# Kernel optimization log

Hardware: AMD Instinct MI355X
Metric: run time of the kernel (lower is better)

## Reference

```python
import jax, jax.numpy as jnp
import numpy as np

B, C, H, W = 2, 256, 64, 64
NUM_HEADS = 4
HEAD_DIM = C // NUM_HEADS
N = H * W


def setup_inputs() -> dict:
    key = jax.random.key(0)
    ks = jax.random.split(key, 10)
    x = jax.random.normal(ks[0], (B, C, H, W), dtype=jnp.float32)
    # mostly-True mask; diagonal forced True so every row has a valid key
    m = jax.random.uniform(ks[1], (B, N, N)) > 0.1
    spatial_mask = m | jnp.eye(N, dtype=bool)[None]
    s = 1.0 / np.sqrt(C)
    wq = jax.random.normal(ks[2], (C, C), dtype=jnp.float32) * s
    bq = jnp.zeros((C,), jnp.float32)
    wk = jax.random.normal(ks[3], (C, C), dtype=jnp.float32) * s
    bk = jnp.zeros((C,), jnp.float32)
    wv = jax.random.normal(ks[4], (C, C), dtype=jnp.float32) * s
    bv = jnp.zeros((C,), jnp.float32)
    # torch zero-inits out_proj; use random weights for a non-trivial baseline
    wo = jax.random.normal(ks[5], (C, C), dtype=jnp.float32) * s
    bo = jnp.zeros((C,), jnp.float32)
    return {"x": x, "spatial_mask": spatial_mask, "wq": wq, "bq": bq,
            "wk": wk, "bk": bk, "wv": wv, "bv": bv, "wo": wo, "bo": bo}


def reference(x, spatial_mask, wq, bq, wk, bk, wv, bv, wo, bo):
    b, c, h, w = x.shape
    n = h * w
    nh, hd = NUM_HEADS, HEAD_DIM
    scale = hd ** -0.5
    x_flat = x.reshape(b, c, n).transpose(0, 2, 1)           # [b, n, c]
    q = (x_flat @ wq.T + bq).reshape(b, n, nh, hd).transpose(0, 2, 1, 3)
    k = (x_flat @ wk.T + bk).reshape(b, n, nh, hd).transpose(0, 2, 1, 3)
    v = (x_flat @ wv.T + bv).reshape(b, n, nh, hd).transpose(0, 2, 1, 3)
    logits = jnp.einsum('bhqd,bhkd->bhqk', q, k) * scale      # [b, nh, n, n]
    logits = jnp.where(spatial_mask[:, None], logits, -jnp.inf)
    attn = jax.nn.softmax(logits, axis=-1)                    # dropout = identity (eval)
    out = jnp.einsum('bhqk,bhkd->bhqd', attn, v)              # [b, nh, n, hd]
    out = out.transpose(0, 2, 1, 3).reshape(b, n, c)
    out = out @ wo.T + bo
    return out.transpose(0, 2, 1).reshape(b, c, h, w)
```

## Files before the change

kernel.cpp:

```cpp
#include <hip/hip_runtime.h>
#include <math.h>

namespace {
constexpr int B_    = 2;
constexpr int C_    = 256;
constexpr int NHEAD = 4;
constexpr int HDIM  = 64;
constexpr int NTOK  = 4096;
constexpr float SCALE = 0.125f;
constexpr float LOG2E = 1.44269504f;
}

typedef _Float16 half8  __attribute__((ext_vector_type(8)));
typedef _Float16 half4  __attribute__((ext_vector_type(4)));
typedef __fp16   fp16x2 __attribute__((ext_vector_type(2)));
typedef float    floatx4 __attribute__((ext_vector_type(4)));
typedef int      int4v   __attribute__((ext_vector_type(4)));
typedef unsigned int uint2v __attribute__((ext_vector_type(2)));

__device__ __forceinline__ void plswap32(int &a, int &b) {
#if __has_builtin(__builtin_amdgcn_permlane32_swap)
    const uint2v r = __builtin_amdgcn_permlane32_swap((unsigned)a, (unsigned)b, false, false);
    a = (int)r[0]; b = (int)r[1];
#else
    asm volatile("s_nop 1\n\tv_permlane32_swap_b32 %0, %1\n\ts_nop 1"
                 : "+v"(a), "+v"(b));
#endif
}
__device__ __forceinline__ void plswap16(int &a, int &b) {
#if __has_builtin(__builtin_amdgcn_permlane16_swap)
    const uint2v r = __builtin_amdgcn_permlane16_swap((unsigned)a, (unsigned)b, false, false);
    a = (int)r[0]; b = (int)r[1];
#else
    asm volatile("s_nop 1\n\tv_permlane16_swap_b32 %0, %1\n\ts_nop 1"
                 : "+v"(a), "+v"(b));
#endif
}

__device__ __forceinline__ void gload_lds16(const _Float16* g, _Float16* l, int lane) {
#if __has_builtin(__builtin_amdgcn_global_load_lds)
    __builtin_amdgcn_global_load_lds(
        (const __attribute__((address_space(1))) void*)g,
        (__attribute__((address_space(3))) void*)l, 16, 0, 0);
#else
    *(half8*)((char*)l + lane * 16) = *(const half8*)g;
#endif
}

__global__ __launch_bounds__(256) void wprep(
    const float* __restrict__ wq, const float* __restrict__ wk,
    const float* __restrict__ wv, const float* __restrict__ wo,
    _Float16* __restrict__ w16)
{
    const float* src = (blockIdx.y == 0) ? wq :
                       (blockIdx.y == 1) ? wk :
                       (blockIdx.y == 2) ? wv : wo;
    const int i8 = (blockIdx.x * 256 + threadIdx.x) * 8;
    const float4 a = *(const float4*)&src[i8];
    const float4 b = *(const float4*)&src[i8 + 4];
    half8 h;
    h[0]=(_Float16)a.x; h[1]=(_Float16)a.y; h[2]=(_Float16)a.z; h[3]=(_Float16)a.w;
    h[4]=(_Float16)b.x; h[5]=(_Float16)b.y; h[6]=(_Float16)b.z; h[7]=(_Float16)b.w;
    *(half8*)&w16[(size_t)blockIdx.y * 65536 + i8] = h;
}

__global__ __launch_bounds__(256) void pack_mask(
    const unsigned int* __restrict__ m32, unsigned int* __restrict__ packed)
{
    int c0 = 0, c1 = 0, c2 = 0, c3 = 0;
    #pragma unroll
    for (int i = 0; i < 16; i++) {
        const unsigned int d = m32[i];
        c0 += (d == 0x00000001u);
        c1 += (d == 0x3F803F80u);
        c2 += (d == 0x3F800000u);
        c3 += (d == 0x01010101u);
    }
    int fmt = 1, best = c1;
    if (c0 > best) { best = c0; fmt = 0; }
    if (c2 > best) { best = c2; fmt = 2; }
    if (c3 > best) { best = c3; fmt = 3; }

    const unsigned int W = blockIdx.x * 256 + threadIdx.x;
    unsigned int bits = 0;
    if (fmt == 1) {
        const uint4* p4 = (const uint4*)(m32 + (size_t)W * 16);
        #pragma unroll
        for (int i = 0; i < 4; i++) {
            const uint4 v = p4[i];
            const unsigned int d[4] = { v.x, v.y, v.z, v.w };
            #pragma unroll
            for (int j = 0; j < 4; j++) {
                const int e = i * 8 + j * 2;
                bits |= ((d[j] & 0xFFFFu) ? 1u : 0u) << e;
                bits |= ((d[j] >> 16)     ? 1u : 0u) << (e + 1);
            }
        }
    } else if (fmt != 3) {
        const uint4* p4 = (const uint4*)(m32 + (size_t)W * 32);
        #pragma unroll
        for (int i = 0; i < 8; i++) {
            const uint4 v = p4[i];
            bits |= (v.x ? 1u : 0u) << (i * 4 + 0);
            bits |= (v.y ? 1u : 0u) << (i * 4 + 1);
            bits |= (v.z ? 1u : 0u) << (i * 4 + 2);
            bits |= (v.w ? 1u : 0u) << (i * 4 + 3);
        }
    } else {
        const uint4* p4 = (const uint4*)(m32 + (size_t)W * 8);
        #pragma unroll
        for (int i = 0; i < 2; i++) {
            const uint4 v = p4[i];
            const unsigned int d[4] = { v.x, v.y, v.z, v.w };
            #pragma unroll
            for (int j = 0; j < 4; j++) {
                const int e = (i * 4 + j) * 4;
                bits |= ((d[j] & 0x000000FFu) ? 1u : 0u) << (e + 0);
                bits |= ((d[j] & 0x0000FF00u) ? 1u : 0u) << (e + 1);
                bits |= ((d[j] & 0x00FF0000u) ? 1u : 0u) << (e + 2);
                bits |= ((d[j] & 0xFF000000u) ? 1u : 0u) << (e + 3);
            }
        }
    }
    packed[W] = bits;
}

__global__ __launch_bounds__(256) void qkv_mfma(
    const float* __restrict__ x, const _Float16* __restrict__ w16,
    const float* __restrict__ bq, const float* __restrict__ bk,
    const float* __restrict__ bv,
    _Float16* __restrict__ qo, _Float16* __restrict__ ko,
    _Float16* __restrict__ vo)
{
    const int nt = blockIdx.x;
    const int b  = blockIdx.y;
    const int p  = blockIdx.z;

    const _Float16* w = w16 + (size_t)p * C_ * C_;
    const float* bias = (p == 0) ? bq : (p == 1) ? bk : bv;

    const int t    = threadIdx.x;
    const int wid  = t >> 6;
    const int lane = t & 63;
    const int quad = lane >> 4;
    const int l15  = lane & 15;
    const int n0   = nt * 64;

    __shared__ _Float16 xsh[64 * 264];
    __shared__ _Float16 tbuf[64 * 72];

    const int srow = t >> 2;
    const int sc   = (t & 3) * 16;

    {
        const int cr = t >> 4;
        const int nu = (t & 15) * 4;
        const float* xb = x + (size_t)b * C_ * NTOK;
        #pragma unroll
        for (int cc = 0; cc < 16; cc++) {
            const int cl = cc * 16 + cr;
            const float4 v = *(const float4*)&xb[(size_t)cl * NTOK + n0 + nu];
            xsh[(nu + 0) * 264 + cl] = (_Float16)v.x;
            xsh[(nu + 1) * 264 + cl] = (_Float16)v.y;
            xsh[(nu + 2) * 264 + cl] = (_Float16)v.z;
            xsh[(nu + 3) * 264 + cl] = (_Float16)v.w;
        }
    }
    __syncthreads();

    const _Float16* wrow = &w[(size_t)(wid * 16 + l15) * C_];

    for (int h = 0; h < NHEAD; h++) {
        const int co0 = h * 64;
        floatx4 acc[4];
        #pragma unroll
        for (int i = 0; i < 4; i++) acc[i] = (floatx4)0.f;

        #pragma unroll
        for (int c0 = 0; c0 < C_; c0 += 64) {
            const half8 a0 = *(const half8*)&wrow[(size_t)co0 * C_ + c0 + quad * 8];
            const half8 a1 = *(const half8*)&wrow[(size_t)co0 * C_ + c0 + 32 + quad * 8];
            #pragma unroll
            for (int nt2 = 0; nt2 < 4; nt2++) {
                const half8 b0 = *(const half8*)&xsh[(nt2 * 16 + l15) * 264 + c0 + quad * 8];
                const half8 b1 = *(const half8*)&xsh[(nt2 * 16 + l15) * 264 + c0 + 32 + quad * 8];
                acc[nt2] = __builtin_amdgcn_mfma_f32_16x16x32_f16(a0, b0, acc[nt2], 0, 0, 0);
                acc[nt2] = __builtin_amdgcn_mfma_f32_16x16x32_f16(a1, b1, acc[nt2], 0, 0, 0);
            }
        }

        const float4 bb4 = *(const float4*)&bias[co0 + wid * 16 + quad * 4];
        const float bb[4] = { bb4.x, bb4.y, bb4.z, bb4.w };

        if (p < 2) {
            const float osc = (p == 0) ? (SCALE * LOG2E) : 1.0f;
            #pragma unroll
            for (int nt2 = 0; nt2 < 4; nt2++) {
                half4 hv;
                #pragma unroll
                for (int i = 0; i < 4; i++)
                    hv[i] = (_Float16)((acc[nt2][i] + bb[i]) * osc);
                *(half4*)&tbuf[(nt2 * 16 + l15) * 72 + wid * 16 + quad * 4] = hv;
            }
            __syncthreads();
            _Float16* dh = (p == 0 ? qo : ko) + (size_t)(b * NHEAD + h) * NTOK * HDIM;
            const half8 o0 = *(const half8*)&tbuf[srow * 72 + sc];
            const half8 o1 = *(const half8*)&tbuf[srow * 72 + sc + 8];
            *(half8*)&dh[(size_t)(n0 + srow) * HDIM + sc]     = o0;
            *(half8*)&dh[(size_t)(n0 + srow) * HDIM + sc + 8] = o1;
        } else {
            #pragma unroll
            for (int nt2 = 0; nt2 < 4; nt2++)
                #pragma unroll
                for (int i = 0; i < 4; i++)
                    tbuf[(wid * 16 + quad * 4 + i) * 72 + nt2 * 16 + l15] =
                        (_Float16)(acc[nt2][i] + bb[i]);
            __syncthreads();
            _Float16* vth = vo + (size_t)(b * NHEAD + h) * HDIM * NTOK;
            const half8 o0 = *(const half8*)&tbuf[srow * 72 + sc];
            const half8 o1 = *(const half8*)&tbuf[srow * 72 + sc + 8];
            *(half8*)&vth[(size_t)srow * NTOK + n0 + sc]     = o0;
            *(half8*)&vth[(size_t)srow * NTOK + n0 + sc + 8] = o1;
        }
        __syncthreads();
    }
}

__global__ __launch_bounds__(512) void attn(
    const _Float16* __restrict__ q, const _Float16* __restrict__ k,
    const _Float16* __restrict__ vt, const unsigned int* __restrict__ mpacked,
    _Float16* __restrict__ ao)
{
    const int b  = blockIdx.z;
    const int h  = blockIdx.y;
    const int q0 = blockIdx.x * 128;
    const int t    = threadIdx.x;
    const int w    = t >> 6;
    const int lane = t & 63;
    const int quad = lane >> 4;
    const int l15  = lane & 15;
    const int half = w >> 2;
    const int w4   = w & 3;
    const int koff = half * (NTOK / 2);

    __shared__ __align__(16) char smem_raw[65536];
    _Float16* const sbase = (_Float16*)(smem_raw + half * 32768);

    const size_t head_off = (size_t)(b * NHEAD + h) * NTOK * HDIM;
    const _Float16* qb  = q  + head_off;
    const _Float16* kb  = k  + head_off;
    const _Float16* vtb = vt + head_off;
    const unsigned int* mrow = mpacked + (size_t)b * NTOK * 128;

    const int qrowa = q0 + w4 * 16 + l15;
    const int qrowb = qrowa + 64;
    const half8 aq0a = *(const half8*)&qb[(size_t)qrowa * HDIM + quad * 8];
    const half8 aq1a = *(const half8*)&qb[(size_t)qrowa * HDIM + 32 + quad * 8];
    const half8 aq0b = *(const half8*)&qb[(size_t)qrowb * HDIM + quad * 8];
    const half8 aq1b = *(const half8*)&qb[(size_t)qrowb * HDIM + 32 + quad * 8];
    const unsigned int* mqa = &mrow[(size_t)qrowa * 128];
    const unsigned int* mqb = &mrow[(size_t)qrowb * 128];

    const int jr  = l15 & 7;
    const int xs0 = (quad ^ jr) << 3;
    const int xs1 = ((quad + 4) ^ jr) << 3;

    uint2 mwa = *(const uint2*)&mqa[koff >> 5];
    uint2 mwb = *(const uint2*)&mqb[koff >> 5];
    uint2 mwa_nxt = mwa, mwb_nxt = mwb;

    float l_a = 0.f, l_b = 0.f;
    floatx4 oacca[4], oaccb[4];
    #pragma unroll
    for (int i = 0; i < 4; i++) { oacca[i] = (floatx4)0.f; oaccb[i] = (floatx4)0.f; }

#define STAGE(WO, K0N)                                                        \
    {                                                                         \
        const int rl = lane >> 3;                       \
        const int xc = ((lane & 7) ^ rl) << 3;        \
        const int c0 = w4 * 2, c1 = c0 + 1;                                   \
        gload_lds16(&kb[(size_t)((K0N) + c0 * 8 + rl) * HDIM + xc],           \
                    &sbase[(WO) + c0 * 512], lane);                           \
        gload_lds16(&kb[(size_t)((K0N) + c1 * 8 + rl) * HDIM + xc],           \
                    &sbase[(WO) + c1 * 512], lane);                           \
        gload_lds16(&vtb[(size_t)(c0 * 8 + rl) * NTOK + (K0N) + xc],          \
                    &sbase[(WO) + 4096 + c0 * 512], lane);                    \
        gload_lds16(&vtb[(size_t)(c1 * 8 + rl) * NTOK + (K0N) + xc],          \
                    &sbase[(WO) + 4096 + c1 * 512], lane);                    \
    }

    STAGE(0, koff)
    __syncthreads();

#define SOFTMAX_CT(SA, CT, WORD, SH, LL, Pa, Pb)                                  \
    {                                                                             \
        const unsigned nib = ((WORD) >> ((SH) + quad * 4)) & 0xFu;                \
        const float p0 = __builtin_amdgcn_exp2f((nib & 1u) ? SA[CT][0] : -3.0e38f);\
        const float p1 = __builtin_amdgcn_exp2f((nib & 2u) ? SA[CT][1] : -3.0e38f);\
        const float p2 = __builtin_amdgcn_exp2f((nib & 4u) ? SA[CT][2] : -3.0e38f);\
        const float p3 = __builtin_amdgcn_exp2f((nib & 8u) ? SA[CT][3] : -3.0e38f);\
        LL += (p0 + p1) + (p2 + p3);                                              \
        Pa = __builtin_bit_cast(int, __builtin_amdgcn_cvt_pkrtz(p0, p1));         \
        Pb = __builtin_bit_cast(int, __builtin_amdgcn_cvt_pkrtz(p2, p3));         \
    }

#define ATTN_TILE(RO, WO, KT, PF)                                                 \
    {                                                                             \
        if (PF) {                                                                 \
            const int k0n = koff + (KT) * 64 + 64;                                \
            STAGE(WO, k0n)                                                        \
            mwa_nxt = *(const uint2*)&mqa[k0n >> 5];                              \
            mwb_nxt = *(const uint2*)&mqb[k0n >> 5];                              \
        }                                                                         \
        floatx4 saa[4], sab[4];                                                   \
        __builtin_amdgcn_s_setprio(1);                                            \
        _Pragma("unroll")                                                         \
        for (int ct = 0; ct < 4; ct++) {                                          \
            saa[ct] = (floatx4)0.f; sab[ct] = (floatx4)0.f;                       \
            const half8 ka0 = *(const half8*)&sbase[(RO) + (ct*16 + l15)*64 + xs0];\
            const half8 ka1 = *(const half8*)&sbase[(RO) + (ct*16 + l15)*64 + xs1];\
            saa[ct] = __builtin_amdgcn_mfma_f32_16x16x32_f16(ka0, aq0a, saa[ct], 0, 0, 0); \
            saa[ct] = __builtin_amdgcn_mfma_f32_16x16x32_f16(ka1, aq1a, saa[ct], 0, 0, 0); \
            sab[ct] = __builtin_amdgcn_mfma_f32_16x16x32_f16(ka0, aq0b, sab[ct], 0, 0, 0); \
            sab[ct] = __builtin_amdgcn_mfma_f32_16x16x32_f16(ka1, aq1b, sab[ct], 0, 0, 0); \
        }                                                                         \
        __builtin_amdgcn_s_setprio(0);                                            \
        int A00,A01,A10,A11,A20,A21,A30,A31;                                      \
        int B00,B01,B10,B11,B20,B21,B30,B31;                                      \
        SOFTMAX_CT(saa, 0, mwa.x, 0,  l_a, A00, A01)                              \
        SOFTMAX_CT(saa, 1, mwa.x, 16, l_a, A10, A11)                              \
        SOFTMAX_CT(saa, 2, mwa.y, 0,  l_a, A20, A21)                              \
        SOFTMAX_CT(saa, 3, mwa.y, 16, l_a, A30, A31)                              \
        SOFTMAX_CT(sab, 0, mwb.x, 0,  l_b, B00, B01)                              \
        SOFTMAX_CT(sab, 1, mwb.x, 16, l_b, B10, B11)                              \
        SOFTMAX_CT(sab, 2, mwb.y, 0,  l_b, B20, B21)                              \
        SOFTMAX_CT(sab, 3, mwb.y, 16, l_b, B30, B31)                              \
        mwa = mwa_nxt; mwb = mwb_nxt;                                             \
        plswap32(A00, A10); plswap32(A01, A11);                                   \
        plswap32(A20, A30); plswap32(A21, A31);                                   \
        plswap16(A00, A10); plswap16(A01, A11);                                   \
        plswap16(A20, A30); plswap16(A21, A31);                                   \
        plswap32(B00, B10); plswap32(B01, B11);                                   \
        plswap32(B20, B30); plswap32(B21, B31);                                   \
        plswap16(B00, B10); plswap16(B01, B11);                                   \
        plswap16(B20, B30); plswap16(B21, B31);                                   \
        const half8 pb0a = __builtin_bit_cast(half8, (int4v){A00, A01, A10, A11});\
        const half8 pb1a = __builtin_bit_cast(half8, (int4v){A20, A21, A30, A31});\
        const half8 pb0b = __builtin_bit_cast(half8, (int4v){B00, B01, B10, B11});\
        const half8 pb1b = __builtin_bit_cast(half8, (int4v){B20, B21, B30, B31});\
        __builtin_amdgcn_s_setprio(1);                                            \
        _Pragma("unroll")                                                         \
        for (int dt = 0; dt < 4; dt++) {                                          \
            const half8 va0 = *(const half8*)&sbase[(RO) + 4096 + (dt*16 + l15)*64 + xs0];\
            const half8 va1 = *(const half8*)&sbase[(RO) + 4096 + (dt*16 + l15)*64 + xs1];\
            oacca[dt] = __builtin_amdgcn_mfma_f32_16x16x32_f16(va0, pb0a, oacca[dt], 0, 0, 0); \
            oacca[dt] = __builtin_amdgcn_mfma_f32_16x16x32_f16(va1, pb1a, oacca[dt], 0, 0, 0); \
            oaccb[dt] = __builtin_amdgcn_mfma_f32_16x16x32_f16(va0, pb0b, oaccb[dt], 0, 0, 0); \
            oaccb[dt] = __builtin_amdgcn_mfma_f32_16x16x32_f16(va1, pb1b, oaccb[dt], 0, 0, 0); \
        }                                                                         \
        __builtin_amdgcn_s_setprio(0);                                            \
        __syncthreads();                                                          \
    }

    for (int kt2 = 0; kt2 < 15; kt2++) {
        ATTN_TILE(0,    8192, 2 * kt2,     1)
        ATTN_TILE(8192, 0,    2 * kt2 + 1, 1)
    }
    ATTN_TILE(0,    8192, 30, 1)
    ATTN_TILE(8192, 0,    31, 0)

#undef ATTN_TILE
#undef SOFTMAX_CT
#undef STAGE

    l_a += __shfl_xor(l_a, 16, 64);
    l_a += __shfl_xor(l_a, 32, 64);
    l_b += __shfl_xor(l_b, 16, 64);
    l_b += __shfl_xor(l_b, 32, 64);

    __syncthreads();
    float* oex = (float*)smem_raw;
    float* lex = (float*)(smem_raw + 32768);
    if (w >= 4) {
        float* dst = &oex[((size_t)(w - 4) * 64 + lane) * 32];
        #pragma unroll
        for (int dt = 0; dt < 4; dt++) {
            *(floatx4*)&dst[dt * 4]      = oacca[dt];
            *(floatx4*)&dst[16 + dt * 4] = oaccb[dt];
        }
        if (quad == 0) {
            lex[(w - 4) * 16 + l15]      = l_a;
            lex[64 + (w - 4) * 16 + l15] = l_b;
        }
    }
    __syncthreads();
    if (w < 4) {
        const float* src = &oex[((size_t)w * 64 + lane) * 32];
        const float lta = l_a + lex[w * 16 + l15];
        const float ltb = l_b + lex[64 + w * 16 + l15];
        const float inva = (lta > 0.f) ? (1.0f / lta) : 0.f;
        const float invb = (ltb > 0.f) ? (1.0f / ltb) : 0.f;
        _Float16* aoba = ao + ((size_t)b * NTOK + q0 + w * 16 + l15) * C_ + h * 64;
        _Float16* aobb = ao + ((size_t)b * NTOK + q0 + 64 + w * 16 + l15) * C_ + h * 64;
        #pragma unroll
        for (int dt = 0; dt < 4; dt++) {
            const floatx4 o2a = *(const floatx4*)&src[dt * 4];
            const floatx4 o2b = *(const floatx4*)&src[16 + dt * 4];
            half4 ra, rb;
            #pragma unroll
            for (int rr = 0; rr < 4; rr++) {
                ra[rr] = (_Float16)((oacca[dt][rr] + o2a[rr]) * inva);
                rb[rr] = (_Float16)((oaccb[dt][rr] + o2b[rr]) * invb);
            }
            *(half4*)&aoba[dt * 16 + quad * 4] = ra;
            *(half4*)&aobb[dt * 16 + quad * 4] = rb;
        }
    }
}

__global__ __launch_bounds__(256) void out_mfma(
    const _Float16* __restrict__ ao, const _Float16* __restrict__ wo16,
    const float* __restrict__ bo, float* __restrict__ out)
{
    const int nt  = blockIdx.x;
    const int cot = blockIdx.y;
    const int b   = blockIdx.z;
    const int t    = threadIdx.x;
    const int wid  = t >> 6;
    const int lane = t & 63;
    const int quad = lane >> 4;
    const int l15  = lane & 15;
    const int n0  = nt * 64;
    const int co0 = cot * 64;

    __shared__ float tf[64 * 68];

    floatx4 acc[4];
    #pragma unroll
    for (int i = 0; i < 4; i++) acc[i] = (floatx4)0.f;

    const _Float16* wrow = &wo16[(size_t)(co0 + wid * 16 + l15) * C_];
    const _Float16* aob  = ao + ((size_t)b * NTOK + n0) * C_;

    #pragma unroll
    for (int c0 = 0; c0 < C_; c0 += 64) {
        const half8 a0 = *(const half8*)&wrow[c0 + quad * 8];
        const half8 a1 = *(const half8*)&wrow[c0 + 32 + quad * 8];
        #pragma unroll
        for (int nt2 = 0; nt2 < 4; nt2++) {
            const half8 b0 = *(const half8*)&aob[(size_t)(nt2 * 16 + l15) * C_ + c0 + quad * 8];
            const half8 b1 = *(const half8*)&aob[(size_t)(nt2 * 16 + l15) * C_ + c0 + 32 + quad * 8];
            acc[nt2] = __builtin_amdgcn_mfma_f32_16x16x32_f16(a0, b0, acc[nt2], 0, 0, 0);
            acc[nt2] = __builtin_amdgcn_mfma_f32_16x16x32_f16(a1, b1, acc[nt2], 0, 0, 0);
        }
    }

    #pragma unroll
    for (int nt2 = 0; nt2 < 4; nt2++)
        #pragma unroll
        for (int i = 0; i < 4; i++)
            tf[(wid * 16 + quad * 4 + i) * 68 + nt2 * 16 + l15] = acc[nt2][i];
    __syncthreads();

    const int row = t >> 2;
    const int c4  = (t & 3) * 16;
    const float bb = bo[co0 + row];
    float* orow = &out[((size_t)(b * C_ + co0 + row)) * NTOK + n0 + c4];
    #pragma unroll
    for (int u = 0; u < 4; u++) {
        float4 v = *(const float4*)&tf[row * 68 + c4 + u * 4];
        v.x += bb; v.y += bb; v.z += bb; v.w += bb;
        *(float4*)&orow[u * 4] = v;
    }
}

extern "C" void kernel_launch(void* const* d_in, const int* in_sizes, int n_in,
                              void* d_out, int out_size, void* d_ws, size_t ws_size,
                              hipStream_t stream) {
    const float* x    = (const float*)d_in[0];
    const void*  mask = d_in[1];
    const float* wq   = (const float*)d_in[2];
    const float* bq   = (const float*)d_in[3];
    const float* wk   = (const float*)d_in[4];
    const float* bk   = (const float*)d_in[5];
    const float* wv   = (const float*)d_in[6];
    const float* bv   = (const float*)d_in[7];
    const float* wo   = (const float*)d_in[8];
    const float* bo   = (const float*)d_in[9];
    float* out = (float*)d_out;

    const size_t qkv_elems = (size_t)B_ * NHEAD * NTOK * HDIM;
    _Float16* wsh = (_Float16*)d_ws;
    _Float16* qbuf  = wsh;
    _Float16* kbuf  = wsh + qkv_elems;
    _Float16* vtbuf = wsh + 2 * qkv_elems;
    _Float16* aobuf = wsh + 3 * qkv_elems;
    unsigned int* mpacked = (unsigned int*)(wsh + 4 * qkv_elems);
    _Float16* w16buf = wsh + 4 * qkv_elems + 2 * (size_t)(B_ * NTOK * 128);

    wprep<<<dim3(32, 4), 256, 0, stream>>>(wq, wk, wv, wo, w16buf);
    pack_mask<<<dim3((B_ * NTOK * 128) / 256), 256, 0, stream>>>(
        (const unsigned int*)mask, mpacked);
    qkv_mfma<<<dim3(NTOK / 64, B_, 3), 256, 0, stream>>>(
        x, w16buf, bq, bk, bv, qbuf, kbuf, vtbuf);
    attn<<<dim3(NTOK / 128, NHEAD, B_), 512, 0, stream>>>(
        qbuf, kbuf, vtbuf, mpacked, aobuf);
    out_mfma<<<dim3(NTOK / 64, C_ / 64, B_), 256, 0, stream>>>(
        aobuf, w16buf + 3 * 65536, bo, out);
}
```

Before: 292.1 us.

## Fuse weight prep, mask packing and QKV projection into one launch

Drops the separate weight-conversion kernel and has the QKV and output projections read fp32 weights directly, converting them to fp16 in registers. The mask-packing kernel is merged into the QKV launch as extra blocks, so two fewer kernel launches and their serialization gaps remain. In exchange, weight loads now fetch twice the bytes and convert on every use. Mask-packing blocks share a grid with the MFMA blocks, which changes scheduling.

```diff
diff --git a/kernel.cpp b/kernel.cpp
--- a/kernel.cpp
+++ b/kernel.cpp
@@ -9,6 +9,7 @@
 constexpr int NTOK  = 4096;
 constexpr float SCALE = 0.125f;
 constexpr float LOG2E = 1.44269504f;
+constexpr int QKV_BLOCKS = 3 * B_ * (NTOK / 64);
 }
 
 typedef _Float16 half8  __attribute__((ext_vector_type(8)));
@@ -47,96 +48,91 @@
 #endif
 }
 
-__global__ __launch_bounds__(256) void wprep(
-    const float* __restrict__ wq, const float* __restrict__ wk,
-    const float* __restrict__ wv, const float* __restrict__ wo,
-    _Float16* __restrict__ w16)
-{
-    const float* src = (blockIdx.y == 0) ? wq :
-                       (blockIdx.y == 1) ? wk :
-                       (blockIdx.y == 2) ? wv : wo;
-    const int i8 = (blockIdx.x * 256 + threadIdx.x) * 8;
-    const float4 a = *(const float4*)&src[i8];
-    const float4 b = *(const float4*)&src[i8 + 4];
+__device__ __forceinline__ half8 ldcvt8(const float* p) {
+    const float4 a = *(const float4*)p;
+    const float4 b = *(const float4*)(p + 4);
     half8 h;
     h[0]=(_Float16)a.x; h[1]=(_Float16)a.y; h[2]=(_Float16)a.z; h[3]=(_Float16)a.w;
     h[4]=(_Float16)b.x; h[5]=(_Float16)b.y; h[6]=(_Float16)b.z; h[7]=(_Float16)b.w;
-    *(half8*)&w16[(size_t)blockIdx.y * 65536 + i8] = h;
-}
-
-__global__ __launch_bounds__(256) void pack_mask(
-    const unsigned int* __restrict__ m32, unsigned int* __restrict__ packed)
-{
-    int c0 = 0, c1 = 0, c2 = 0, c3 = 0;
-    #pragma unroll
-    for (int i = 0; i < 16; i++) {
-        const unsigned int d = m32[i];
-        c0 += (d == 0x00000001u);
-        c1 += (d == 0x3F803F80u);
-        c2 += (d == 0x3F800000u);
-        c3 += (d == 0x01010101u);
-    }
-    int fmt = 1, best = c1;
-    if (c0 > best) { best = c0; fmt = 0; }
-    if (c2 > best) { best = c2; fmt = 2; }
-    if (c3 > best) { best = c3; fmt = 3; }
-
-    const unsigned int W = blockIdx.x * 256 + threadIdx.x;
-    unsigned int bits = 0;
-    if (fmt == 1) {
-        const uint4* p4 = (const uint4*)(m32 + (size_t)W * 16);
-        #pragma unroll
-        for (int i = 0; i < 4; i++) {
-            const uint4 v = p4[i];
-            const unsigned int d[4] = { v.x, v.y, v.z, v.w };
-            #pragma unroll
-            for (int j = 0; j < 4; j++) {
-                const int e = i * 8 + j * 2;
-                bits |= ((d[j] & 0xFFFFu) ? 1u : 0u) << e;
-                bits |= ((d[j] >> 16)     ? 1u : 0u) << (e + 1);
-            }
-        }
-    } else if (fmt != 3) {
-        const uint4* p4 = (const uint4*)(m32 + (size_t)W * 32);
-        #pragma unroll
-        for (int i = 0; i < 8; i++) {
-            const uint4 v = p4[i];
-            bits |= (v.x ? 1u : 0u) << (i * 4 + 0);
-            bits |= (v.y ? 1u : 0u) << (i * 4 + 1);
-            bits |= (v.z ? 1u : 0u) << (i * 4 + 2);
-            bits |= (v.w ? 1u : 0u) << (i * 4 + 3);
-        }
-    } else {
-        const uint4* p4 = (const uint4*)(m32 + (size_t)W * 8);
-        #pragma unroll
-        for (int i = 0; i < 2; i++) {
-            const uint4 v = p4[i];
-            const unsigned int d[4] = { v.x, v.y, v.z, v.w };
-            #pragma unroll
-            for (int j = 0; j < 4; j++) {
-                const int e = (i * 4 + j) * 4;
-                bits |= ((d[j] & 0x000000FFu) ? 1u : 0u) << (e + 0);
-                bits |= ((d[j] & 0x0000FF00u) ? 1u : 0u) << (e + 1);
-                bits |= ((d[j] & 0x00FF0000u) ? 1u : 0u) << (e + 2);
-                bits |= ((d[j] & 0xFF000000u) ? 1u : 0u) << (e + 3);
-            }
-        }
-    }
-    packed[W] = bits;
-}
-
-__global__ __launch_bounds__(256) void qkv_mfma(
-    const float* __restrict__ x, const _Float16* __restrict__ w16,
+    return h;
+}
+
+__global__ __launch_bounds__(256) void qkv_pack(
+    const float* __restrict__ x,
+    const float* __restrict__ wq, const float* __restrict__ wk,
+    const float* __restrict__ wv,
     const float* __restrict__ bq, const float* __restrict__ bk,
     const float* __restrict__ bv,
+    const unsigned int* __restrict__ m32, unsigned int* __restrict__ packed,
     _Float16* __restrict__ qo, _Float16* __restrict__ ko,
     _Float16* __restrict__ vo)
 {
-    const int nt = blockIdx.x;
-    const int b  = blockIdx.y;
-    const int p  = blockIdx.z;
-
-    const _Float16* w = w16 + (size_t)p * C_ * C_;
+    if (blockIdx.x >= QKV_BLOCKS) {
+        int c0 = 0, c1 = 0, c2 = 0, c3 = 0;
+        #pragma unroll
+        for (int i = 0; i < 16; i++) {
+            const unsigned int d = m32[i];
+            c0 += (d == 0x00000001u);
+            c1 += (d == 0x3F803F80u);
+            c2 += (d == 0x3F800000u);
+            c3 += (d == 0x01010101u);
+        }
+        int fmt = 1, best = c1;
+        if (c0 > best) { best = c0; fmt = 0; }
+        if (c2 > best) { best = c2; fmt = 2; }
+        if (c3 > best) { best = c3; fmt = 3; }
+
+        const unsigned int W = (blockIdx.x - QKV_BLOCKS) * 256 + threadIdx.x;
+        unsigned int bits = 0;
+        if (fmt == 1) {
+            const uint4* p4 = (const uint4*)(m32 + (size_t)W * 16);
+            #pragma unroll
+            for (int i = 0; i < 4; i++) {
+                const uint4 v = p4[i];
+                const unsigned int d[4] = { v.x, v.y, v.z, v.w };
+                #pragma unroll
+                for (int j = 0; j < 4; j++) {
+                    const int e = i * 8 + j * 2;
+                    bits |= ((d[j] & 0xFFFFu) ? 1u : 0u) << e;
+                    bits |= ((d[j] >> 16)     ? 1u : 0u) << (e + 1);
+                }
+            }
+        } else if (fmt != 3) {
+            const uint4* p4 = (const uint4*)(m32 + (size_t)W * 32);
+            #pragma unroll
+            for (int i = 0; i < 8; i++) {
+                const uint4 v = p4[i];
+                bits |= (v.x ? 1u : 0u) << (i * 4 + 0);
+                bits |= (v.y ? 1u : 0u) << (i * 4 + 1);
+                bits |= (v.z ? 1u : 0u) << (i * 4 + 2);
+                bits |= (v.w ? 1u : 0u) << (i * 4 + 3);
+            }
+        } else {
+            const uint4* p4 = (const uint4*)(m32 + (size_t)W * 8);
+            #pragma unroll
+            for (int i = 0; i < 2; i++) {
+                const uint4 v = p4[i];
+                const unsigned int d[4] = { v.x, v.y, v.z, v.w };
+                #pragma unroll
+                for (int j = 0; j < 4; j++) {
+                    const int e = (i * 4 + j) * 4;
+                    bits |= ((d[j] & 0x000000FFu) ? 1u : 0u) << (e + 0);
+                    bits |= ((d[j] & 0x0000FF00u) ? 1u : 0u) << (e + 1);
+                    bits |= ((d[j] & 0x00FF0000u) ? 1u : 0u) << (e + 2);
+                    bits |= ((d[j] & 0xFF000000u) ? 1u : 0u) << (e + 3);
+                }
+            }
+        }
+        packed[W] = bits;
+        return;
+    }
+
+    const int bid = blockIdx.x;
+    const int p   = bid >> 7;
+    const int b   = (bid >> 6) & 1;
+    const int nt  = bid & 63;
+
+    const float* w    = (p == 0) ? wq : (p == 1) ? wk : wv;
     const float* bias = (p == 0) ? bq : (p == 1) ? bk : bv;
 
     const int t    = threadIdx.x;
@@ -168,7 +164,7 @@
     }
     __syncthreads();
 
-    const _Float16* wrow = &w[(size_t)(wid * 16 + l15) * C_];
+    const float* wrow = &w[(size_t)(wid * 16 + l15) * C_];
 
     for (int h = 0; h < NHEAD; h++) {
         const int co0 = h * 64;
@@ -178,8 +174,8 @@
 
         #pragma unroll
         for (int c0 = 0; c0 < C_; c0 += 64) {
-            const half8 a0 = *(const half8*)&wrow[(size_t)co0 * C_ + c0 + quad * 8];
-            const half8 a1 = *(const half8*)&wrow[(size_t)co0 * C_ + c0 + 32 + quad * 8];
+            const half8 a0 = ldcvt8(&wrow[(size_t)co0 * C_ + c0 + quad * 8]);
+            const half8 a1 = ldcvt8(&wrow[(size_t)co0 * C_ + c0 + 32 + quad * 8]);
             #pragma unroll
             for (int nt2 = 0; nt2 < 4; nt2++) {
                 const half8 b0 = *(const half8*)&xsh[(nt2 * 16 + l15) * 264 + c0 + quad * 8];
@@ -419,7 +415,7 @@
 }
 
 __global__ __launch_bounds__(256) void out_mfma(
-    const _Float16* __restrict__ ao, const _Float16* __restrict__ wo16,
+    const _Float16* __restrict__ ao, const float* __restrict__ wo,
     const float* __restrict__ bo, float* __restrict__ out)
 {
     const int nt  = blockIdx.x;
@@ -439,13 +435,13 @@
     #pragma unroll
     for (int i = 0; i < 4; i++) acc[i] = (floatx4)0.f;
 
-    const _Float16* wrow = &wo16[(size_t)(co0 + wid * 16 + l15) * C_];
+    const float* wrow = &wo[(size_t)(co0 + wid * 16 + l15) * C_];
     const _Float16* aob  = ao + ((size_t)b * NTOK + n0) * C_;
 
     #pragma unroll
     for (int c0 = 0; c0 < C_; c0 += 64) {
-        const half8 a0 = *(const half8*)&wrow[c0 + quad * 8];
-        const half8 a1 = *(const half8*)&wrow[c0 + 32 + quad * 8];
+        const half8 a0 = ldcvt8(&wrow[c0 + quad * 8]);
+        const half8 a1 = ldcvt8(&wrow[c0 + 32 + quad * 8]);
         #pragma unroll
         for (int nt2 = 0; nt2 < 4; nt2++) {
             const half8 b0 = *(const half8*)&aob[(size_t)(nt2 * 16 + l15) * C_ + c0 + quad * 8];
@@ -496,15 +492,12 @@
     _Float16* vtbuf = wsh + 2 * qkv_elems;
     _Float16* aobuf = wsh + 3 * qkv_elems;
     unsigned int* mpacked = (unsigned int*)(wsh + 4 * qkv_elems);
-    _Float16* w16buf = wsh + 4 * qkv_elems + 2 * (size_t)(B_ * NTOK * 128);
-
-    wprep<<<dim3(32, 4), 256, 0, stream>>>(wq, wk, wv, wo, w16buf);
-    pack_mask<<<dim3((B_ * NTOK * 128) / 256), 256, 0, stream>>>(
-        (const unsigned int*)mask, mpacked);
-    qkv_mfma<<<dim3(NTOK / 64, B_, 3), 256, 0, stream>>>(
-        x, w16buf, bq, bk, bv, qbuf, kbuf, vtbuf);
+
+    qkv_pack<<<dim3(QKV_BLOCKS + (B_ * NTOK * 128) / 256), 256, 0, stream>>>(
+        x, wq, wk, wv, bq, bk, bv,
+        (const unsigned int*)mask, mpacked, qbuf, kbuf, vtbuf);
     attn<<<dim3(NTOK / 128, NHEAD, B_), 512, 0, stream>>>(
         qbuf, kbuf, vtbuf, mpacked, aobuf);
     out_mfma<<<dim3(NTOK / 64, C_ / 64, B_), 256, 0, stream>>>(
-        aobuf, w16buf + 3 * 65536, bo, out);
-}
+        aobuf, wo, bo, out);
+}
```

Result: faster. 284.2 us (median of 2 runs) (-2.7%).
